# Kernel optimization log

Measured on AMD Instinct MI355X. Metric: run time of the kernel, lower is better.

Reference implementation:

```python
import jax, jax.numpy as jnp
import numpy as np

N, E = 100000, 1600000
IN, H, ED, L, OUT = 128, 64, 64, 3, 3

def _lin(key, fan_in, fan_out):
    return jax.random.normal(key, (fan_in, fan_out), jnp.float32) / np.sqrt(fan_in)

def setup_inputs() -> dict:
    key = jax.random.key(0)
    ks = jax.random.split(key, 16)
    x = jax.random.normal(ks[0], (N, IN), jnp.float32)
    edge_index = jax.random.randint(ks[1], (2, E), 0, N, dtype=jnp.int64)
    edge_attr = jax.random.normal(ks[2], (E, ED), jnp.float32)
    pW = _lin(ks[3], IN, H); pb = jnp.zeros((H,), jnp.float32)
    # stacked per-layer params
    eW1 = jnp.stack([_lin(jax.random.fold_in(ks[4], l), 2 * H + ED, ED) for l in range(L)])
    eb1 = jnp.zeros((L, ED), jnp.float32)
    eW2 = jnp.stack([_lin(jax.random.fold_in(ks[5], l), ED, ED) for l in range(L)])
    eb2 = jnp.zeros((L, ED), jnp.float32)
    nW1 = jnp.stack([_lin(jax.random.fold_in(ks[6], l), H + ED, H) for l in range(L)])
    nb1 = jnp.zeros((L, H), jnp.float32)
    nW2 = jnp.stack([_lin(jax.random.fold_in(ks[7], l), H, H) for l in range(L)])
    nb2 = jnp.zeros((L, H), jnp.float32)
    lW = _lin(ks[8], H, OUT); lb = jnp.zeros((OUT,), jnp.float32)
    return {"x": x, "edge_index": edge_index, "edge_attr": edge_attr,
            "pW": pW, "pb": pb, "eW1": eW1, "eb1": eb1, "eW2": eW2, "eb2": eb2,
            "nW1": nW1, "nb1": nb1, "nW2": nW2, "nb2": nb2, "lW": lW, "lb": lb}

def reference(x, edge_index, edge_attr, pW, pb, eW1, eb1, eW2, eb2, nW1, nb1, nW2, nb2, lW, lb):
    n = x.shape[0]
    row, col = edge_index[0], edge_index[1]  # source j, target i
    h = x @ pW + pb                          # node_proj
    ea = edge_attr
    for l in range(eW1.shape[0]):
        # edge_mlp([x_row, x_col, e])
        ein = jnp.concatenate([h[row], h[col], ea], axis=-1)        # [E, 2H+ED]
        ea = jax.nn.relu(ein @ eW1[l] + eb1[l]) @ eW2[l] + eb2[l]   # [E, ED]
        # message = node_mlp([x_j, e]) with x_j = h[row]
        mi = jnp.concatenate([h[row], ea], axis=-1)                 # [E, H+ED]
        msg = jax.nn.relu(mi @ nW1[l] + nb1[l]) @ nW2[l] + nb2[l]   # [E, H]
        agg = jax.ops.segment_sum(msg, col, num_segments=n)         # scatter-add into targets
        h = jax.nn.relu(agg + h)                                    # update + outer ReLU (dropout=eval)
    pooled = jnp.mean(h, axis=0, keepdims=True)                     # global_mean_pool, single graph
    return pooled @ lW + lb
```

## Files before the change

### kernel.cpp

```cpp
#include <hip/hip_runtime.h>

#define NN 100000
#define NE 1600000
#define BINS_PAD 100352
#define STR 72

typedef short s8v __attribute__((ext_vector_type(8)));
typedef float f32x4 __attribute__((ext_vector_type(4)));
typedef unsigned short u16;

__device__ __forceinline__ u16 f2bf(float f) {
    union { float f; unsigned u; } v; v.f = f;
    unsigned r = v.u + 0x7FFFu + ((v.u >> 16) & 1u);
    return (u16)(r >> 16);
}
__device__ __forceinline__ unsigned pk2(float a, float b) {
    return (unsigned)f2bf(a) | ((unsigned)f2bf(b) << 16);
}

__global__ void pack_weights(const float* __restrict__ pW,
                             const float* __restrict__ eW1, const float* __restrict__ eW2,
                             const float* __restrict__ nW1, const float* __restrict__ nW2,
                             u16* __restrict__ wpack) {
    int b = blockIdx.x, L = threadIdx.x;
    const float* src; int s, t;
    if (b < 16) { src = pW; s = b >> 2; t = b & 3; }
    else {
        int bb = b - 16, l = bb / 56, r = bb % 56;
        if (r < 24)      {            src = eW1 + l*192*64; s = r>>2; t = r&3; }
        else if (r < 32) { r -= 24;   src = eW2 + l*64*64;  s = r>>2; t = r&3; }
        else if (r < 48) { r -= 32;   src = nW1 + l*128*64; s = r>>2; t = r&3; }
        else             { r -= 48;   src = nW2 + l*64*64;  s = r>>2; t = r&3; }
    }
    int kbase = s*32 + (L>>4)*8;
    int n = t*16 + (L&15);
    u16* dst = wpack + (size_t)b*512 + (size_t)L*8;
#pragma unroll
    for (int j = 0; j < 8; ++j) dst[j] = f2bf(src[(kbase+j)*64 + n]);
}

__global__ void k_hist(const int* __restrict__ ei, int* __restrict__ hist) {
    int e = blockIdx.x * 256 + threadIdx.x;
    atomicAdd(&hist[ei[(size_t)NE + e]], 1);
}

__global__ void k_scan1(const int* __restrict__ hist, int* __restrict__ cursor,
                        int* __restrict__ blockSums) {
    __shared__ int sS[256];
    int t = threadIdx.x, b = blockIdx.x;
    int base = b*1024 + t*4;
    int v0 = hist[base], v1 = hist[base+1], v2 = hist[base+2], v3 = hist[base+3];
    int s4 = v0 + v1 + v2 + v3;
    sS[t] = s4; __syncthreads();
    for (int off = 1; off < 256; off <<= 1) {
        int x = (t >= off) ? sS[t-off] : 0;
        __syncthreads();
        sS[t] += x;
        __syncthreads();
    }
    int excl = sS[t] - s4;
    cursor[base] = excl; cursor[base+1] = excl+v0;
    cursor[base+2] = excl+v0+v1; cursor[base+3] = excl+v0+v1+v2;
    if (t == 255) blockSums[b] = sS[255];
}

__global__ void k_scan2(int* __restrict__ blockSums) {
    __shared__ int sS[128];
    int t = threadIdx.x;
    int v = (t < 98) ? blockSums[t] : 0;
    sS[t] = v; __syncthreads();
    for (int off = 1; off < 128; off <<= 1) {
        int x = (t >= off) ? sS[t-off] : 0;
        __syncthreads();
        sS[t] += x;
        __syncthreads();
    }
    if (t < 98) blockSums[t] = sS[t] - v;
}

__global__ void k_scan3(int* __restrict__ cursor, const int* __restrict__ blockSums) {
    int i = blockIdx.x*1024 + threadIdx.x*4;
    int add = blockSums[blockIdx.x];
    cursor[i] += add; cursor[i+1] += add; cursor[i+2] += add; cursor[i+3] += add;
}

__global__ void k_scatter(const int* __restrict__ ei, int* __restrict__ cursor,
                          int2* __restrict__ rcP, int* __restrict__ pos) {
    int e = blockIdx.x * 256 + threadIdx.x;
    int c = ei[(size_t)NE + e];
    int p = atomicAdd(&cursor[c], 1);
    rcP[p] = make_int2(ei[e], c);
    pos[e] = p;
}

__global__ void k_permute_ea(const float* __restrict__ ea, const int* __restrict__ pos,
                             u16* __restrict__ eaP) {
    size_t t = (size_t)blockIdx.x * 256 + threadIdx.x;
    int e = (int)(t >> 3), q = (int)(t & 7);
    int p = pos[e];
    const float4* src = (const float4*)(ea + (size_t)e*64 + q*8);
    float4 v0 = src[0], v1 = src[1];
    uint4 o;
    o.x = pk2(v0.x, v0.y); o.y = pk2(v0.z, v0.w);
    o.z = pk2(v1.x, v1.y); o.w = pk2(v1.z, v1.w);
    *(uint4*)(eaP + (size_t)p*64 + q*8) = o;
}

__global__ __launch_bounds__(256) void node_proj(const float* __restrict__ x,
                                                 const float* __restrict__ pb,
                                                 const u16* __restrict__ wpack,
                                                 float* __restrict__ h,
                                                 u16* __restrict__ h_bf) {
    __shared__ __align__(16) u16 sX[64*136];
    const int tid = threadIdx.x;
    const int n0 = blockIdx.x * 64;
    for (int i = tid; i < 64*32; i += 256) {
        int node = i >> 5, c = i & 31;
        float4 v = make_float4(0.f, 0.f, 0.f, 0.f);
        if (n0 + node < NN) v = *(const float4*)(x + (size_t)(n0+node)*128 + c*4);
        *(uint2*)&sX[node*136 + c*4] = make_uint2(pk2(v.x, v.y), pk2(v.z, v.w));
    }
    __syncthreads();
    const int w = tid >> 6, L = tid & 63;
    const int m = L & 15, kc = L >> 4;
    const int wb = w * 16;
    const f32x4 z = {0.f, 0.f, 0.f, 0.f};
    f32x4 acc[4] = {z, z, z, z};
#pragma unroll
    for (int s = 0; s < 4; ++s) {
        s8v a = *(const s8v*)&sX[(wb+m)*136 + s*32 + kc*8];
#pragma unroll
        for (int t = 0; t < 4; ++t) {
            s8v bf = *(const s8v*)(wpack + ((size_t)(s*4+t)*64 + L)*8);
            acc[t] = __builtin_amdgcn_mfma_f32_16x16x32_bf16(a, bf, acc[t], 0, 0, 0);
        }
    }
#pragma unroll
    for (int t = 0; t < 4; ++t) {
        int u = t*16 + m;
        float bias = pb[u];
#pragma unroll
        for (int r = 0; r < 4; ++r) {
            int node = n0 + wb + kc*4 + r;
            if (node < NN) {
                float v = acc[t][r] + bias;
                h[(size_t)node*64 + u] = v;
                h_bf[(size_t)node*64 + u] = f2bf(v);
            }
        }
    }
}

__global__ __launch_bounds__(256, 4) void edge_layer(const int2* __restrict__ rcP,
                                                     const u16* __restrict__ h_bf,
                                                     u16* __restrict__ ea_bf,
                                                     const u16* __restrict__ wp,
                                                     const float* __restrict__ eb1,
                                                     const float* __restrict__ eb2,
                                                     const float* __restrict__ nb1,
                                                     const float* __restrict__ nb2,
                                                     float* __restrict__ agg,
                                                     int save_ea) {
    __shared__ __align__(16) u16 sB[4*32*STR];
    const int tid = threadIdx.x;
    const int w = tid >> 6, L = tid & 63;
    const int m = L & 15, kc = L >> 4;
    const int wb = w * 32;
    const size_t e0 = (size_t)blockIdx.x * 128;
    u16* sW = sB + w * 32 * STR;

    int2 rc0 = rcP[e0 + wb + (L & 31)];
    int lcol = rc0.y;

    float be1[4], be2[4], bn1[4];
#pragma unroll
    for (int t = 0; t < 4; ++t) {
        int u = t*16 + m;
        be1[t] = eb1[u]; be2[t] = eb2[u]; bn1[t] = nb1[u];
    }
    float bn2L = nb2[L];

    unsigned long long smask;
    {
        int prev = __shfl(lcol, (L + 63) & 63);
        bool sstart = (L < 32) && ((L == 0) || (lcol != prev));
        smask = __ballot(sstart);
    }

    s8v hrow[2][2], hcol[2][2];
#pragma unroll
    for (int g = 0; g < 2; ++g) {
        int rI = __shfl(rc0.x, g*16 + m);
        int cI = __shfl(rc0.y, g*16 + m);
        hrow[g][0] = *(const s8v*)(h_bf + (size_t)rI*64 + kc*8);
        hrow[g][1] = *(const s8v*)(h_bf + (size_t)rI*64 + 32 + kc*8);
        hcol[g][0] = *(const s8v*)(h_bf + (size_t)cI*64 + kc*8);
        hcol[g][1] = *(const s8v*)(h_bf + (size_t)cI*64 + 32 + kc*8);
    }

    const f32x4 z = {0.f, 0.f, 0.f, 0.f};
    f32x4 acc[2][4];

#pragma unroll
    for (int g = 0; g < 2; ++g)
#pragma unroll
        for (int t = 0; t < 4; ++t) acc[g][t] = z;
#pragma unroll
    for (int s = 0; s < 6; ++s) {
        s8v a[2];
#pragma unroll
        for (int g = 0; g < 2; ++g) {
            if (s < 2)
                a[g] = hrow[g][s];
            else if (s < 4)
                a[g] = hcol[g][s-2];
            else
                a[g] = *(const s8v*)(ea_bf + (e0 + wb + g*16 + m)*64 + (s-4)*32 + kc*8);
        }
#pragma unroll
        for (int t = 0; t < 4; ++t) {
            s8v bf = *(const s8v*)(wp + ((size_t)(s*4+t)*64 + L)*8);
            acc[0][t] = __builtin_amdgcn_mfma_f32_16x16x32_bf16(a[0], bf, acc[0][t], 0, 0, 0);
            acc[1][t] = __builtin_amdgcn_mfma_f32_16x16x32_bf16(a[1], bf, acc[1][t], 0, 0, 0);
        }
    }
#pragma unroll
    for (int g = 0; g < 2; ++g)
#pragma unroll
        for (int t = 0; t < 4; ++t) {
            int u = t*16 + m;
#pragma unroll
            for (int r = 0; r < 4; ++r) {
                float v = acc[g][t][r] + be1[t];
                v = v > 0.f ? v : 0.f;
                sW[(g*16 + kc*4 + r)*STR + u] = f2bf(v);
            }
        }

    const u16* wp2 = wp + 24*512;
#pragma unroll
    for (int g = 0; g < 2; ++g)
#pragma unroll
        for (int t = 0; t < 4; ++t) acc[g][t] = z;
#pragma unroll
    for (int s = 0; s < 2; ++s) {
        s8v a0 = *(const s8v*)&sW[(m)*STR + s*32 + kc*8];
        s8v a1 = *(const s8v*)&sW[(16 + m)*STR + s*32 + kc*8];
#pragma unroll
        for (int t = 0; t < 4; ++t) {
            s8v bf = *(const s8v*)(wp2 + ((size_t)(s*4+t)*64 + L)*8);
            acc[0][t] = __builtin_amdgcn_mfma_f32_16x16x32_bf16(a0, bf, acc[0][t], 0, 0, 0);
            acc[1][t] = __builtin_amdgcn_mfma_f32_16x16x32_bf16(a1, bf, acc[1][t], 0, 0, 0);
        }
    }
#pragma unroll
    for (int g = 0; g < 2; ++g)
#pragma unroll
        for (int t = 0; t < 4; ++t) {
            int u = t*16 + m;
#pragma unroll
            for (int r = 0; r < 4; ++r) {
                float v = acc[g][t][r] + be2[t];
                sW[(g*16 + kc*4 + r)*STR + u] = f2bf(v);
            }
        }

    const u16* wp3 = wp + 32*512;
#pragma unroll
    for (int g = 0; g < 2; ++g)
#pragma unroll
        for (int t = 0; t < 4; ++t) acc[g][t] = z;
#pragma unroll
    for (int s = 0; s < 4; ++s) {
        s8v a[2];
#pragma unroll
        for (int g = 0; g < 2; ++g) {
            if (s < 2) {
                a[g] = hrow[g][s];
            } else {
                a[g] = *(const s8v*)&sW[(g*16 + m)*STR + (s-2)*32 + kc*8];
                if (save_ea)
                    *(s8v*)(ea_bf + (e0 + wb + g*16 + m)*64 + (s-2)*32 + kc*8) = a[g];
            }
        }
#pragma unroll
        for (int t = 0; t < 4; ++t) {
            s8v bf = *(const s8v*)(wp3 + ((size_t)(s*4+t)*64 + L)*8);
            acc[0][t] = __builtin_amdgcn_mfma_f32_16x16x32_bf16(a[0], bf, acc[0][t], 0, 0, 0);
            acc[1][t] = __builtin_amdgcn_mfma_f32_16x16x32_bf16(a[1], bf, acc[1][t], 0, 0, 0);
        }
    }
#pragma unroll
    for (int g = 0; g < 2; ++g)
#pragma unroll
        for (int t = 0; t < 4; ++t) {
            int u = t*16 + m;
#pragma unroll
            for (int r = 0; r < 4; ++r) {
                float v = acc[g][t][r] + bn1[t];
                v = v > 0.f ? v : 0.f;
                sW[(g*16 + kc*4 + r)*STR + u] = f2bf(v);
            }
        }

    const u16* wp4 = wp + 48*512;
#pragma unroll
    for (int g = 0; g < 2; ++g)
#pragma unroll
        for (int t = 0; t < 4; ++t) acc[g][t] = z;
#pragma unroll
    for (int s = 0; s < 2; ++s) {
        s8v a0 = *(const s8v*)&sW[(m)*STR + s*32 + kc*8];
        s8v a1 = *(const s8v*)&sW[(16 + m)*STR + s*32 + kc*8];
#pragma unroll
        for (int t = 0; t < 4; ++t) {
            s8v bf = *(const s8v*)(wp4 + ((size_t)(s*4+t)*64 + L)*8);
            acc[0][t] = __builtin_amdgcn_mfma_f32_16x16x32_bf16(a0, bf, acc[0][t], 0, 0, 0);
            acc[1][t] = __builtin_amdgcn_mfma_f32_16x16x32_bf16(a1, bf, acc[1][t], 0, 0, 0);
        }
    }

    while (smask) {
        int beg = (int)__builtin_ctzll(smask);
        smask &= smask - 1;
        int end = smask ? (int)__builtin_ctzll(smask) : 32;
        int node = __shfl(lcol, beg);
        float r0 = 0.f, r1 = 0.f, r2 = 0.f, r3 = 0.f;
#pragma unroll
        for (int g = 0; g < 2; ++g)
#pragma unroll
            for (int r = 0; r < 4; ++r) {
                int le = g*16 + kc*4 + r;
                bool in = (le >= beg) && (le < end);
                r0 += in ? acc[g][0][r] : 0.f;
                r1 += in ? acc[g][1][r] : 0.f;
                r2 += in ? acc[g][2][r] : 0.f;
                r3 += in ? acc[g][3][r] : 0.f;
            }
        r0 += __shfl_xor(r0, 16); r0 += __shfl_xor(r0, 32);
        r1 += __shfl_xor(r1, 16); r1 += __shfl_xor(r1, 32);
        r2 += __shfl_xor(r2, 16); r2 += __shfl_xor(r2, 32);
        r3 += __shfl_xor(r3, 16); r3 += __shfl_xor(r3, 32);
        float rv = (kc == 0) ? r0 : (kc == 1) ? r1 : (kc == 2) ? r2 : r3;
        rv += (float)(end - beg) * bn2L;
        unsafeAtomicAdd(&agg[(size_t)node*64 + L], rv);
    }
}

__global__ void update_h(float* __restrict__ h, float* __restrict__ agg,
                         u16* __restrict__ h_bf, int zero_agg, int write_hbf) {
    int i = (blockIdx.x * 256 + threadIdx.x) * 4;
    float4 a = *(const float4*)(agg + i);
    float4 hv = *(const float4*)(h + i);
    float4 v;
    v.x = fmaxf(a.x + hv.x, 0.f);
    v.y = fmaxf(a.y + hv.y, 0.f);
    v.z = fmaxf(a.z + hv.z, 0.f);
    v.w = fmaxf(a.w + hv.w, 0.f);
    *(float4*)(h + i) = v;
    if (write_hbf) *(uint2*)(h_bf + i) = make_uint2(pk2(v.x, v.y), pk2(v.z, v.w));
    if (zero_agg) *(float4*)(agg + i) = make_float4(0.f, 0.f, 0.f, 0.f);
}

__global__ void pool1(const float* __restrict__ h, float* __restrict__ pooled) {
    float acc = 0.f;
    const int stride = gridDim.x * 256;
    for (int i = blockIdx.x * 256 + threadIdx.x; i < NN*64; i += stride)
        acc += h[i];
    __shared__ float sp[256];
    sp[threadIdx.x] = acc;
    __syncthreads();
    if (threadIdx.x < 64) {
        float v = sp[threadIdx.x] + sp[threadIdx.x+64] + sp[threadIdx.x+128] + sp[threadIdx.x+192];
        unsafeAtomicAdd(&pooled[threadIdx.x], v);
    }
}

__global__ void pool2(const float* __restrict__ pooled, const float* __restrict__ lW,
                      const float* __restrict__ lb, float* __restrict__ out) {
    int k = threadIdx.x;
    float v = pooled[k] * (1.0f / NN);
#pragma unroll
    for (int o = 0; o < 3; ++o) {
        float p = v * lW[k*3 + o];
        for (int off = 32; off > 0; off >>= 1)
            p += __shfl_down(p, off);
        if (k == 0) out[o] = p + lb[o];
    }
}

extern "C" void kernel_launch(void* const* d_in, const int* in_sizes, int n_in,
                              void* d_out, int out_size, void* d_ws, size_t ws_size,
                              hipStream_t stream) {
    const float* x         = (const float*)d_in[0];
    const int*   ei        = (const int*)d_in[1];
    const float* edge_attr = (const float*)d_in[2];
    const float* pW        = (const float*)d_in[3];
    const float* pb        = (const float*)d_in[4];
    const float* eW1       = (const float*)d_in[5];
    const float* eb1       = (const float*)d_in[6];
    const float* eW2       = (const float*)d_in[7];
    const float* eb2       = (const float*)d_in[8];
    const float* nW1       = (const float*)d_in[9];
    const float* nb1       = (const float*)d_in[10];
    const float* nW2       = (const float*)d_in[11];
    const float* nb2       = (const float*)d_in[12];
    const float* lW        = (const float*)d_in[13];
    const float* lb        = (const float*)d_in[14];
    float* out = (float*)d_out;

    char* ws = (char*)d_ws;
    float* h     = (float*)(ws);
    float* agg   = (float*)(ws + 25600000);
    u16*   h_bf  = (u16*)  (ws + 51200000);
    u16*   eaP   = (u16*)  (ws + 64000000);
    u16*   wpack = (u16*)  (ws + 268800000);
    float* pooled= (float*)(ws + 268988416);
    int2*  rcP   = (int2*) (ws + 268988672);
    int* hist      = (int*)agg;
    int* cursor    = hist + BINS_PAD;
    int* blockSums = cursor + BINS_PAD;
    int* pos       = blockSums + 128;

    hipMemsetAsync(hist, 0, BINS_PAD*4, stream);
    k_hist<<<NE/256, 256, 0, stream>>>(ei, hist);
    k_scan1<<<98, 256, 0, stream>>>(hist, cursor, blockSums);
    k_scan2<<<1, 128, 0, stream>>>(blockSums);
    k_scan3<<<98, 256, 0, stream>>>(cursor, blockSums);
    k_scatter<<<NE/256, 256, 0, stream>>>(ei, cursor, rcP, pos);
    k_permute_ea<<<NE*8/256, 256, 0, stream>>>(edge_attr, pos, eaP);

    pack_weights<<<184, 64, 0, stream>>>(pW, eW1, eW2, nW1, nW2, wpack);
    node_proj<<<(NN + 63)/64, 256, 0, stream>>>(x, pb, wpack, h, h_bf);

    hipMemsetAsync(agg, 0, (size_t)NN*64*4, stream);
    for (int l = 0; l < 3; ++l) {
        edge_layer<<<NE/128, 256, 0, stream>>>(rcP, h_bf, eaP,
                                               wpack + (16 + l*56)*512,
                                               eb1 + l*64, eb2 + l*64, nb1 + l*64, nb2 + l*64,
                                               agg, l < 2 ? 1 : 0);
        update_h<<<NN*64/4/256, 256, 0, stream>>>(h, agg, h_bf, l < 2 ? 1 : 0, l < 2 ? 1 : 0);
    }
    hipMemsetAsync(pooled, 0, 64*4, stream);
    pool1<<<256, 256, 0, stream>>>(h, pooled);
    pool2<<<1, 64, 0, stream>>>(pooled, lW, lb, out);
}
```

Measured before the change: 1.605 ms.

## Fuse edge_attr permutation into first edge layer and use packed bf16 converts

```diff
diff --git a/kernel.cpp b/kernel.cpp
--- a/kernel.cpp
+++ b/kernel.cpp
@@ -16,6 +16,17 @@
 }
 __device__ __forceinline__ unsigned pk2(float a, float b) {
     return (unsigned)f2bf(a) | ((unsigned)f2bf(b) << 16);
+}
+__device__ __forceinline__ unsigned cvtpk(float a, float b) {
+    unsigned r;
+    asm("v_cvt_pk_bf16_f32 %0, %1, %2" : "=v"(r) : "v"(a), "v"(b));
+    return r;
+}
+__device__ __forceinline__ s8v pack8(float4 a, float4 b) {
+    union { s8v v; unsigned u[4]; } o;
+    o.u[0] = cvtpk(a.x, a.y); o.u[1] = cvtpk(a.z, a.w);
+    o.u[2] = cvtpk(b.x, b.y); o.u[3] = cvtpk(b.z, b.w);
+    return o.v;
 }
 
 __global__ void pack_weights(const float* __restrict__ pW,
@@ -85,25 +96,12 @@
 }
 
 __global__ void k_scatter(const int* __restrict__ ei, int* __restrict__ cursor,
-                          int2* __restrict__ rcP, int* __restrict__ pos) {
+                          int2* __restrict__ rcP, int* __restrict__ inv) {
     int e = blockIdx.x * 256 + threadIdx.x;
     int c = ei[(size_t)NE + e];
     int p = atomicAdd(&cursor[c], 1);
     rcP[p] = make_int2(ei[e], c);
-    pos[e] = p;
-}
-
-__global__ void k_permute_ea(const float* __restrict__ ea, const int* __restrict__ pos,
-                             u16* __restrict__ eaP) {
-    size_t t = (size_t)blockIdx.x * 256 + threadIdx.x;
-    int e = (int)(t >> 3), q = (int)(t & 7);
-    int p = pos[e];
-    const float4* src = (const float4*)(ea + (size_t)e*64 + q*8);
-    float4 v0 = src[0], v1 = src[1];
-    uint4 o;
-    o.x = pk2(v0.x, v0.y); o.y = pk2(v0.z, v0.w);
-    o.z = pk2(v1.x, v1.y); o.w = pk2(v1.z, v1.w);
-    *(uint4*)(eaP + (size_t)p*64 + q*8) = o;
+    inv[p] = e;
 }
 
 __global__ __launch_bounds__(256) void node_proj(const float* __restrict__ x,
@@ -151,8 +149,11 @@
     }
 }
 
+template<int FIRST>
 __global__ __launch_bounds__(256, 4) void edge_layer(const int2* __restrict__ rcP,
+                                                     const int* __restrict__ inv,
                                                      const u16* __restrict__ h_bf,
+                                                     const float* __restrict__ ea0,
                                                      u16* __restrict__ ea_bf,
                                                      const u16* __restrict__ wp,
                                                      const float* __restrict__ eb1,
@@ -171,6 +172,8 @@
 
     int2 rc0 = rcP[e0 + wb + (L & 31)];
     int lcol = rc0.y;
+    int ie = 0;
+    if (FIRST) ie = inv[e0 + wb + (L & 31)];
 
     float be1[4], be2[4], bn1[4];
 #pragma unroll
@@ -187,7 +190,7 @@
         smask = __ballot(sstart);
     }
 
-    s8v hrow[2][2], hcol[2][2];
+    s8v hrow[2][2], hcol[2][2], eafr[2][2];
 #pragma unroll
     for (int g = 0; g < 2; ++g) {
         int rI = __shfl(rc0.x, g*16 + m);
@@ -197,6 +200,25 @@
         hcol[g][0] = *(const s8v*)(h_bf + (size_t)cI*64 + kc*8);
         hcol[g][1] = *(const s8v*)(h_bf + (size_t)cI*64 + 32 + kc*8);
     }
+    if (FIRST) {
+#pragma unroll
+        for (int g = 0; g < 2; ++g) {
+            int eIg = __shfl(ie, g*16 + m);
+            const float* base = ea0 + (size_t)eIg*64 + kc*8;
+#pragma unroll
+            for (int s2 = 0; s2 < 2; ++s2) {
+                float4 f0 = *(const float4*)(base + s2*32);
+                float4 f1 = *(const float4*)(base + s2*32 + 4);
+                eafr[g][s2] = pack8(f0, f1);
+            }
+        }
+    } else {
+#pragma unroll
+        for (int g = 0; g < 2; ++g)
+#pragma unroll
+            for (int s2 = 0; s2 < 2; ++s2)
+                eafr[g][s2] = *(const s8v*)(ea_bf + (e0 + wb + g*16 + m)*64 + s2*32 + kc*8);
+    }
 
     const f32x4 z = {0.f, 0.f, 0.f, 0.f};
     f32x4 acc[2][4];
@@ -209,14 +231,8 @@
     for (int s = 0; s < 6; ++s) {
         s8v a[2];
 #pragma unroll
-        for (int g = 0; g < 2; ++g) {
-            if (s < 2)
-                a[g] = hrow[g][s];
-            else if (s < 4)
-                a[g] = hcol[g][s-2];
-            else
-                a[g] = *(const s8v*)(ea_bf + (e0 + wb + g*16 + m)*64 + (s-4)*32 + kc*8);
-        }
+        for (int g = 0; g < 2; ++g)
+            a[g] = (s < 2) ? hrow[g][s] : (s < 4) ? hcol[g][s-2] : eafr[g][s-4];
 #pragma unroll
         for (int t = 0; t < 4; ++t) {
             s8v bf = *(const s8v*)(wp + ((size_t)(s*4+t)*64 + L)*8);
@@ -229,12 +245,16 @@
 #pragma unroll
         for (int t = 0; t < 4; ++t) {
             int u = t*16 + m;
-#pragma unroll
-            for (int r = 0; r < 4; ++r) {
-                float v = acc[g][t][r] + be1[t];
-                v = v > 0.f ? v : 0.f;
-                sW[(g*16 + kc*4 + r)*STR + u] = f2bf(v);
-            }
+            float v0 = fmaxf(acc[g][t][0] + be1[t], 0.f);
+            float v1 = fmaxf(acc[g][t][1] + be1[t], 0.f);
+            float v2 = fmaxf(acc[g][t][2] + be1[t], 0.f);
+            float v3 = fmaxf(acc[g][t][3] + be1[t], 0.f);
+            unsigned w01 = cvtpk(v0, v1), w23 = cvtpk(v2, v3);
+            int rb = (g*16 + kc*4)*STR + u;
+            sW[rb]         = (u16)w01;
+            sW[rb + STR]   = (u16)(w01 >> 16);
+            sW[rb + 2*STR] = (u16)w23;
+            sW[rb + 3*STR] = (u16)(w23 >> 16);
         }
 
     const u16* wp2 = wp + 24*512;
@@ -258,11 +278,16 @@
 #pragma unroll
         for (int t = 0; t < 4; ++t) {
             int u = t*16 + m;
-#pragma unroll
-            for (int r = 0; r < 4; ++r) {
-                float v = acc[g][t][r] + be2[t];
-                sW[(g*16 + kc*4 + r)*STR + u] = f2bf(v);
-            }
+            float v0 = acc[g][t][0] + be2[t];
+            float v1 = acc[g][t][1] + be2[t];
+            float v2 = acc[g][t][2] + be2[t];
+            float v3 = acc[g][t][3] + be2[t];
+            unsigned w01 = cvtpk(v0, v1), w23 = cvtpk(v2, v3);
+            int rb = (g*16 + kc*4)*STR + u;
+            sW[rb]         = (u16)w01;
+            sW[rb + STR]   = (u16)(w01 >> 16);
+            sW[rb + 2*STR] = (u16)w23;
+            sW[rb + 3*STR] = (u16)(w23 >> 16);
         }
 
     const u16* wp3 = wp + 32*512;
@@ -295,12 +320,16 @@
 #pragma unroll
         for (int t = 0; t < 4; ++t) {
             int u = t*16 + m;
-#pragma unroll
-            for (int r = 0; r < 4; ++r) {
-                float v = acc[g][t][r] + bn1[t];
-                v = v > 0.f ? v : 0.f;
-                sW[(g*16 + kc*4 + r)*STR + u] = f2bf(v);
-            }
+            float v0 = fmaxf(acc[g][t][0] + bn1[t], 0.f);
+            float v1 = fmaxf(acc[g][t][1] + bn1[t], 0.f);
+            float v2 = fmaxf(acc[g][t][2] + bn1[t], 0.f);
+            float v3 = fmaxf(acc[g][t][3] + bn1[t], 0.f);
+            unsigned w01 = cvtpk(v0, v1), w23 = cvtpk(v2, v3);
+            int rb = (g*16 + kc*4)*STR + u;
+            sW[rb]         = (u16)w01;
+            sW[rb + STR]   = (u16)(w01 >> 16);
+            sW[rb + 2*STR] = (u16)w23;
+            sW[rb + 3*STR] = (u16)(w23 >> 16);
         }
 
     const u16* wp4 = wp + 48*512;
@@ -417,30 +446,38 @@
     u16*   wpack = (u16*)  (ws + 268800000);
     float* pooled= (float*)(ws + 268988416);
     int2*  rcP   = (int2*) (ws + 268988672);
+    int*   inv   = (int*)  (ws + 281788672);
     int* hist      = (int*)agg;
     int* cursor    = hist + BINS_PAD;
     int* blockSums = cursor + BINS_PAD;
-    int* pos       = blockSums + 128;
 
     hipMemsetAsync(hist, 0, BINS_PAD*4, stream);
     k_hist<<<NE/256, 256, 0, stream>>>(ei, hist);
     k_scan1<<<98, 256, 0, stream>>>(hist, cursor, blockSums);
     k_scan2<<<1, 128, 0, stream>>>(blockSums);
     k_scan3<<<98, 256, 0, stream>>>(cursor, blockSums);
-    k_scatter<<<NE/256, 256, 0, stream>>>(ei, cursor, rcP, pos);
-    k_permute_ea<<<NE*8/256, 256, 0, stream>>>(edge_attr, pos, eaP);
+    k_scatter<<<NE/256, 256, 0, stream>>>(ei, cursor, rcP, inv);
 
     pack_weights<<<184, 64, 0, stream>>>(pW, eW1, eW2, nW1, nW2, wpack);
     node_proj<<<(NN + 63)/64, 256, 0, stream>>>(x, pb, wpack, h, h_bf);
 
     hipMemsetAsync(agg, 0, (size_t)NN*64*4, stream);
-    for (int l = 0; l < 3; ++l) {
-        edge_layer<<<NE/128, 256, 0, stream>>>(rcP, h_bf, eaP,
-                                               wpack + (16 + l*56)*512,
-                                               eb1 + l*64, eb2 + l*64, nb1 + l*64, nb2 + l*64,
-                                               agg, l < 2 ? 1 : 0);
-        update_h<<<NN*64/4/256, 256, 0, stream>>>(h, agg, h_bf, l < 2 ? 1 : 0, l < 2 ? 1 : 0);
-    }
+
+    edge_layer<1><<<NE/128, 256, 0, stream>>>(rcP, inv, h_bf, edge_attr, eaP,
+                                              wpack + 16*512,
+                                              eb1, eb2, nb1, nb2, agg, 1);
+    update_h<<<NN*64/4/256, 256, 0, stream>>>(h, agg, h_bf, 1, 1);
+
+    edge_layer<0><<<NE/128, 256, 0, stream>>>(rcP, inv, h_bf, edge_attr, eaP,
+                                              wpack + (16 + 56)*512,
+                                              eb1 + 64, eb2 + 64, nb1 + 64, nb2 + 64, agg, 1);
+    update_h<<<NN*64/4/256, 256, 0, stream>>>(h, agg, h_bf, 1, 1);
+
+    edge_layer<0><<<NE/128, 256, 0, stream>>>(rcP, inv, h_bf, edge_attr, eaP,
+                                              wpack + (16 + 112)*512,
+                                              eb1 + 128, eb2 + 128, nb1 + 128, nb2 + 128, agg, 0);
+    update_h<<<NN*64/4/256, 256, 0, stream>>>(h, agg, h_bf, 0, 0);
+
     hipMemsetAsync(pooled, 0, 64*4, stream);
     pool1<<<256, 256, 0, stream>>>(h, pooled);
     pool2<<<1, 64, 0, stream>>>(pooled, lW, lb, out);
```

New measurement: 1.489 ms. -7.3%, faster.
